# Performance work log

Measured on AMD Instinct MI355X. Metric: run time of the kernel, lower is better.

Reference implementation:

```python
import jax, jax.numpy as jnp
import numpy as np

DELTA_PULL = 0.5
DELTA_PUSH = 1.5
ALPHA, BETA, GAMMA = 1.0, 1.0, 0.001
M, E = 2_000_000, 32
NUM_IDS = 65  # labels 0..64; 0 = background


def setup_inputs() -> dict:
    key = jax.random.key(0)
    k1, k2 = jax.random.split(key)
    embeddings = jax.random.normal(k1, (M, E), dtype=jnp.float32)
    instance_labels = jax.random.randint(k2, (M,), 0, NUM_IDS, dtype=jnp.int64)
    return {"embeddings": embeddings, "instance_labels": instance_labels}


def reference(embeddings, instance_labels):
    # Foreground mask; background (label 0) points are excluded from every term.
    fg = instance_labels > 0
    labels = jnp.where(fg, instance_labels, 0).astype(jnp.int32)
    w = fg.astype(embeddings.dtype)  # [M]

    # Per-instance means via one fused segment-sum (replaces Python loop over ids).
    sums = jax.ops.segment_sum(embeddings * w[:, None], labels, num_segments=NUM_IDS)  # [C+1,E]
    counts = jax.ops.segment_sum(w, labels, num_segments=NUM_IDS)                       # [C+1]
    present = (counts > 0).at[0].set(False)  # slot 0 is background
    safe_counts = jnp.maximum(counts, 1.0)
    means = sums / safe_counts[:, None]  # [C+1,E]
    C = jnp.sum(present)
    Cf = jnp.maximum(C, 1).astype(embeddings.dtype)

    # Pull loss: per-point distance to own instance mean, hinged, per-instance mean, then mean over instances.
    diff_pt = embeddings - means[labels]
    d2_pt = jnp.sum(diff_pt * diff_pt, axis=1)
    dist_pt = jnp.sqrt(jnp.where(d2_pt > 0, d2_pt, 1.0))
    dist_pt = jnp.where(d2_pt > 0, dist_pt, 0.0)
    pull_pt = jnp.maximum(dist_pt - DELTA_PULL, 0.0) ** 2 * w
    pull_per_inst = jax.ops.segment_sum(pull_pt, labels, num_segments=NUM_IDS) / safe_counts
    pull_loss = jnp.sum(jnp.where(present, pull_per_inst, 0.0)) / Cf

    # Push loss: vectorized O(C^2) pairwise mean distances with upper-triangular mask.
    dm = means[:, None, :] - means[None, :, :]           # [C+1,C+1,E]
    d2 = jnp.sum(dm * dm, axis=-1)                        # [C+1,C+1]
    iu = jnp.triu(jnp.ones((NUM_IDS, NUM_IDS), bool), k=1)
    pairmask = iu & present[:, None] & present[None, :]
    pd = jnp.sqrt(jnp.where(pairmask, d2, 1.0))
    push = jnp.where(pairmask, jnp.maximum(2.0 * DELTA_PUSH - pd, 0.0) ** 2, 0.0)
    n_pairs = jnp.sum(pairmask)
    push_loss = jnp.where(
        n_pairs > 0,
        jnp.sum(push) / jnp.maximum(n_pairs, 1).astype(embeddings.dtype),
        0.0,
    )

    # Regularizer: mean norm of present instance means.
    mn2 = jnp.sum(means * means, axis=-1)
    mnorm = jnp.sqrt(jnp.where(present, mn2, 1.0))
    reg_loss = jnp.sum(jnp.where(present, mnorm, 0.0)) / Cf

    total = ALPHA * pull_loss + BETA * push_loss + GAMMA * reg_loss
    # If there are no foreground points, loss is 0 (matches torch early-return).
    total = jnp.where(C > 0, total, 0.0)
    return total
```

## Files before the change

### kernel.cpp

```cpp
#include <hip/hip_runtime.h>

#define NUM_IDS 65
#define EDIM 32
#define NSUM (NUM_IDS * EDIM)
#define NTOT (NSUM + NUM_IDS)
#define LPAD 33
#define R36 36
#define CP (NUM_IDS * R36)

#define WS_MEANS   0
#define WS_COEF    2080
#define WS_SUMS    2145
#define WS_PUSH    4290
#define WS_REG     4291
#define WS_CF      4292
#define WS_C       4293
#define WS_PULLACC 4294
#define WS_PART    4352

__global__ void k0_zero(float* __restrict__ ws) {
    int i = blockIdx.x * 256 + threadIdx.x;
    if (i < NTOT) ws[WS_SUMS + i] = 0.f;
}

__global__ __launch_bounds__(256) void k1_reduce(const float4* __restrict__ emb4,
                                                 const int* __restrict__ lab,
                                                 float* __restrict__ ws,
                                                 int M, int nb1, int atomic_mode) {
    __shared__ float ls[4 * CP];
    const int t = threadIdx.x;
    const int wave = t >> 6, lane = t & 63;
    const int s = lane >> 3;
    const int c = lane & 7;
    float* my = ls + wave * CP;
    for (int j = t; j < 4 * CP; j += 256) ls[j] = 0.f;
    __syncthreads();

    float cntreg = 0.f;
    const int lp1 = lane + 1;

    const long stride = (long)nb1 * 32;
    const long p0 = (long)blockIdx.x * 32 + wave * 8 + s;

    auto LD = [&](long p, int& L, float4& v) {
        if (p < M) { L = lab[p]; v = emb4[p * 8 + c]; }
        else       { L = 0; v = make_float4(0.f, 0.f, 0.f, 0.f); }
    };

    auto PR = [&](int L, float4 v) {
        const int off = L * R36 + 4 * c;
        float4 old = *(float4*)(my + off);
        const bool act = (L > 0);
        int key = act ? L : (-64 - s);
        int q0 = __shfl(key, 0 + c),  q1 = __shfl(key, 8 + c);
        int q2 = __shfl(key, 16 + c), q3 = __shfl(key, 24 + c);
        int q4 = __shfl(key, 32 + c), q5 = __shfl(key, 40 + c);
        int q6 = __shfl(key, 48 + c), q7 = __shfl(key, 56 + c);
        cntreg += (float)((q0 == lp1) + (q1 == lp1) + (q2 == lp1) + (q3 == lp1) +
                          (q4 == lp1) + (q5 == lp1) + (q6 == lp1) + (q7 == lp1));
        int ne = 0;
        ne += (0 < s && q0 == key); ne += (1 < s && q1 == key);
        ne += (2 < s && q2 == key); ne += (3 < s && q3 == key);
        ne += (4 < s && q4 == key); ne += (5 < s && q5 == key);
        ne += (6 < s && q6 == key);
        if (act && ne == 0) {
            float4 nv; nv.x = old.x + v.x; nv.y = old.y + v.y;
            nv.z = old.z + v.z; nv.w = old.w + v.w;
            *(float4*)(my + off) = nv;
        }
        if (__ballot(act && ne > 0)) {
            #pragma unroll 1
            for (int r = 1; r < 8; ++r) {
                if (!__ballot(act && ne == r)) break;
                if (act && ne == r) {
                    float4 o2 = *(float4*)(my + off);
                    o2.x += v.x; o2.y += v.y; o2.z += v.z; o2.w += v.w;
                    *(float4*)(my + off) = o2;
                }
            }
        }
    };

    int La, Lb; float4 va, vb;
    long pA = p0;
    LD(pA, La, va);
    while (pA < M) {
        const long pB = pA + stride;
        LD(pB, Lb, vb);
        PR(La, va);
        const long pA2 = pB + stride;
        LD(pA2, La, va);
        PR(Lb, vb);
        pA = pA2;
    }

    my[lp1 * R36 + 32] += cntreg;
    __syncthreads();

    for (int j = t; j < NTOT; j += 256) {
        int off = (j < NSUM) ? ((j >> 5) * R36 + (j & 31))
                             : ((j - NSUM) * R36 + 32);
        float v = ls[off] + ls[CP + off] + ls[2 * CP + off] + ls[3 * CP + off];
        if (atomic_mode) {
            if (v != 0.f) atomicAdd(&ws[WS_SUMS + j], v);
        } else {
            ws[WS_PART + (size_t)blockIdx.x * NTOT + j] = v;
        }
    }
}

__global__ __launch_bounds__(256) void k2_reduce_partials(float* __restrict__ ws, int nb1) {
    const int t = threadIdx.x;
    const int jl = t & 31, bl = t >> 5;
    const int j = blockIdx.x * 32 + jl;
    const float* part = ws + WS_PART;
    float acc = 0.f;
    if (j < NTOT)
        for (int b = bl; b < nb1; b += 8) acc += part[(size_t)b * NTOT + j];
    __shared__ float red[256];
    red[t] = acc;
    __syncthreads();
    for (int sd = 128; sd >= 32; sd >>= 1) {
        if (t < sd) red[t] += red[t + sd];
        __syncthreads();
    }
    if (t < 32) {
        int jj = blockIdx.x * 32 + t;
        if (jj < NTOT) ws[WS_SUMS + jj] = red[t];
    }
}

__global__ __launch_bounds__(256) void k3_finalize(float* __restrict__ ws) {
    __shared__ float lmean[NUM_IDS * LPAD];
    __shared__ float lcnt[NUM_IDS];
    __shared__ int   lpres[NUM_IDS];
    __shared__ float red[256];
    __shared__ float red2[256];
    const int t = threadIdx.x;
    const float* sg = ws + WS_SUMS;

    if (t < NUM_IDS) {
        float cv = sg[NSUM + t];
        lcnt[t] = cv;
        lpres[t] = (t > 0 && cv > 0.f) ? 1 : 0;
    }
    __syncthreads();

    for (int j = t; j < NSUM; j += 256) {
        int cc = j >> 5, e = j & 31;
        float m = sg[j] / fmaxf(lcnt[cc], 1.f);
        ws[WS_MEANS + j] = m;
        lmean[cc * LPAD + e] = m;
    }
    if (t < NUM_IDS) ws[WS_COEF + t] = lpres[t] ? (1.f / fmaxf(lcnt[t], 1.f)) : 0.f;
    __syncthreads();

    float psum = 0.f;
    for (int pi = t; pi < 2080; pi += 256) {
        int i = 0, rem = pi;
        while (rem >= NUM_IDS - 1 - i) { rem -= NUM_IDS - 1 - i; ++i; }
        int jj = i + 1 + rem;
        if (lpres[i] && lpres[jj]) {
            float d2 = 0.f;
            #pragma unroll
            for (int e = 0; e < EDIM; ++e) {
                float d = lmean[i * LPAD + e] - lmean[jj * LPAD + e];
                d2 += d * d;
            }
            float pd = sqrtf(d2);
            float h = fmaxf(3.0f - pd, 0.f);
            psum += h * h;
        }
    }
    float rsum = 0.f;
    if (t < NUM_IDS && lpres[t]) {
        float m2 = 0.f;
        #pragma unroll
        for (int e = 0; e < EDIM; ++e) { float m = lmean[t * LPAD + e]; m2 += m * m; }
        rsum = sqrtf(m2);
    }
    red[t] = psum; red2[t] = rsum;
    __syncthreads();
    for (int sd = 128; sd > 0; sd >>= 1) {
        if (t < sd) { red[t] += red[t + sd]; red2[t] += red2[t + sd]; }
        __syncthreads();
    }
    if (t == 0) {
        int C = 0;
        for (int cc = 1; cc < NUM_IDS; ++cc) C += lpres[cc];
        float Cf = fmaxf((float)C, 1.f);
        long np = (long)C * (C - 1) / 2;
        ws[WS_PUSH] = (np > 0) ? red[0] / (float)np : 0.f;
        ws[WS_REG]  = red2[0] / Cf;
        ws[WS_CF]   = Cf;
        ws[WS_C]    = (float)C;
        ws[WS_PULLACC] = 0.f;
    }
}

__global__ __launch_bounds__(256) void k4_pull(const float4* __restrict__ emb4,
                                               const int* __restrict__ lab,
                                               float* __restrict__ ws,
                                               int M, int nb4) {
    __shared__ float lmean[NUM_IDS * LPAD];
    __shared__ float lcoef[NUM_IDS];
    __shared__ float lpull[NUM_IDS];
    __shared__ float red[NUM_IDS];
    const int t = threadIdx.x;
    for (int j = t; j < NSUM; j += 256) lmean[(j >> 5) * LPAD + (j & 31)] = ws[WS_MEANS + j];
    if (t < NUM_IDS) { lcoef[t] = ws[WS_COEF + t]; lpull[t] = 0.f; }
    __syncthreads();

    const int c = t & 7;
    const long stride = (long)nb4 * 32;
    const long start = (long)blockIdx.x * 32 + (t >> 3);

    auto LD = [&](long p, int& L, float4& v) {
        if (p < M) { L = lab[p]; v = emb4[p * 8 + c]; }
        else       { L = 0; v = make_float4(0.f, 0.f, 0.f, 0.f); }
    };
    auto PR = [&](int L, float4 v) {
        float d2 = 0.f;
        if (L > 0) {
            int bse = L * LPAD + c * 4;
            float dx = v.x - lmean[bse + 0];
            float dy = v.y - lmean[bse + 1];
            float dz = v.z - lmean[bse + 2];
            float dw = v.w - lmean[bse + 3];
            d2 = dx * dx + dy * dy + dz * dz + dw * dw;
        }
        d2 += __shfl_xor(d2, 1);
        d2 += __shfl_xor(d2, 2);
        d2 += __shfl_xor(d2, 4);
        if (c == 0 && L > 0 && d2 > 0.f) {
            float dist = sqrtf(d2);
            float h = fmaxf(dist - 0.5f, 0.f);
            atomicAdd(&lpull[L], h * h);
        }
    };

    int L0, L1;
    float4 v0, v1;
    long pA = start;
    LD(pA, L0, v0);
    while (pA < M) {
        const long pB = pA + stride;
        LD(pB, L1, v1);
        PR(L0, v0);
        const long pA2 = pB + stride;
        LD(pA2, L0, v0);
        PR(L1, v1);
        pA = pA2;
    }
    __syncthreads();
    if (t < NUM_IDS) red[t] = lpull[t] * lcoef[t];
    __syncthreads();
    if (t == 0) {
        float sacc = 0.f;
        for (int cc = 1; cc < NUM_IDS; ++cc) sacc += red[cc];
        atomicAdd(&ws[WS_PULLACC], sacc);
    }
}

__global__ void k5_final(const float* __restrict__ ws, float* __restrict__ out) {
    if (threadIdx.x == 0) {
        float C = ws[WS_C];
        float total = 0.f;
        if (C > 0.f) {
            total = ws[WS_PULLACC] / ws[WS_CF]
                  + ws[WS_PUSH]
                  + 0.001f * ws[WS_REG];
        }
        out[0] = total;
    }
}

extern "C" void kernel_launch(void* const* d_in, const int* in_sizes, int n_in,
                              void* d_out, int out_size, void* d_ws, size_t ws_size,
                              hipStream_t stream) {
    const float4* emb4 = (const float4*)d_in[0];
    const int* lab = (const int*)d_in[1];
    float* ws = (float*)d_ws;
    float* out = (float*)d_out;
    const int M = in_sizes[1];

    long ws_floats = (long)(ws_size / 4);
    long avail = ws_floats - WS_PART - 64;
    int nb1 = (int)(avail / NTOT);
    if (nb1 > 1024) nb1 = 1024;
    int atomic_mode = (nb1 < 8) ? 1 : 0;
    if (atomic_mode) {
        nb1 = 1024;
        k0_zero<<<dim3(9), dim3(256), 0, stream>>>(ws);
    }

    k1_reduce<<<dim3(nb1), dim3(256), 0, stream>>>(emb4, lab, ws, M, nb1, atomic_mode);
    if (!atomic_mode)
        k2_reduce_partials<<<dim3((NTOT + 31) / 32), dim3(256), 0, stream>>>(ws, nb1);
    k3_finalize<<<dim3(1), dim3(256), 0, stream>>>(ws);
    const int nb4 = 2048;
    k4_pull<<<dim3(nb4), dim3(256), 0, stream>>>(emb4, lab, ws, M, nb4);
    k5_final<<<dim3(1), dim3(64), 0, stream>>>(ws, out);
}
```

Before: 169.0 us.

## Triple-buffer loads with inline asm and replace shuffles with DPP in both passes

Both streaming kernels replace the double-buffered load loop with a three-deep software pipeline. Loads are issued as inline-asm global loads with clamped addresses, and explicit vmcnt waits keep several memory requests in flight. The lane layout in the reduce kernel is transposed so the 8 points that collide sit within a DPP row, letting DPP permutes replace ds_bpermute shuffles for duplicate detection and counting. The pull kernel also uses DPP for its 8-lane reduction and float4 mean reads. This risks correctness in the hand-built DPP patterns and vmcnt assumptions, and reads clamped tail elements that are then masked out.

```diff
diff --git a/kernel.cpp b/kernel.cpp
--- a/kernel.cpp
+++ b/kernel.cpp
@@ -18,6 +18,23 @@
 #define WS_PULLACC 4294
 #define WS_PART    4352
 
+#define DPPI(x, ctrl) __builtin_amdgcn_update_dpp(0, (x), (ctrl), 0xF, 0xF, true)
+
+__device__ __forceinline__ void gload4(const float4* p, float4& d) {
+    asm volatile("global_load_dwordx4 %0, %1, off" : "=v"(d) : "v"(p));
+}
+__device__ __forceinline__ void gload1(const int* p, int& d) {
+    asm volatile("global_load_dword %0, %1, off" : "=v"(d) : "v"(p));
+}
+__device__ __forceinline__ void waitN() {
+    asm volatile("s_waitcnt vmcnt(4)" ::: "memory");
+    __builtin_amdgcn_sched_barrier(0);
+}
+__device__ __forceinline__ void wait0() {
+    asm volatile("s_waitcnt vmcnt(0)" ::: "memory");
+    __builtin_amdgcn_sched_barrier(0);
+}
+
 __global__ void k0_zero(float* __restrict__ ws) {
     int i = blockIdx.x * 256 + threadIdx.x;
     if (i < NTOT) ws[WS_SUMS + i] = 0.f;
@@ -26,75 +43,76 @@
 __global__ __launch_bounds__(256) void k1_reduce(const float4* __restrict__ emb4,
                                                  const int* __restrict__ lab,
                                                  float* __restrict__ ws,
-                                                 int M, int nb1, int atomic_mode) {
+                                                 int M, int nb1, int nit, int atomic_mode) {
     __shared__ float ls[4 * CP];
     const int t = threadIdx.x;
     const int wave = t >> 6, lane = t & 63;
-    const int s = lane >> 3;
-    const int c = lane & 7;
+    const int s = lane & 7;
+    const int c = lane >> 3;
     float* my = ls + wave * CP;
     for (int j = t; j < 4 * CP; j += 256) ls[j] = 0.f;
     __syncthreads();
 
-    float cntreg = 0.f;
+    const long Mm1 = (long)M - 1;
+    const long STR = (long)nb1 * 32;
+    const long p0 = (long)blockIdx.x * 32 + wave * 8 + s;
     const int lp1 = lane + 1;
-
-    const long stride = (long)nb1 * 32;
-    const long p0 = (long)blockIdx.x * 32 + wave * 8 + s;
-
-    auto LD = [&](long p, int& L, float4& v) {
-        if (p < M) { L = lab[p]; v = emb4[p * 8 + c]; }
-        else       { L = 0; v = make_float4(0.f, 0.f, 0.f, 0.f); }
+    int cntreg = 0;
+    const int negkey = -64 - s;
+    const int e1 = (s ^ 1) < s, e2 = (s ^ 2) < s, e3 = (s ^ 3) < s,
+              e4 = (s ^ 4) < s, e5 = (s ^ 5) < s, e6 = (s ^ 6) < s, e7 = (s ^ 7) < s;
+
+    auto ISSUE = [&](int j, int& L, float4& v) {
+        long p = p0 + (long)j * STR;
+        long pc = p < Mm1 ? p : Mm1;
+        gload1(lab + pc, L);
+        gload4(emb4 + pc * 8 + c, v);
     };
-
-    auto PR = [&](int L, float4 v) {
-        const int off = L * R36 + 4 * c;
-        float4 old = *(float4*)(my + off);
-        const bool act = (L > 0);
-        int key = act ? L : (-64 - s);
-        int q0 = __shfl(key, 0 + c),  q1 = __shfl(key, 8 + c);
-        int q2 = __shfl(key, 16 + c), q3 = __shfl(key, 24 + c);
-        int q4 = __shfl(key, 32 + c), q5 = __shfl(key, 40 + c);
-        int q6 = __shfl(key, 48 + c), q7 = __shfl(key, 56 + c);
-        cntreg += (float)((q0 == lp1) + (q1 == lp1) + (q2 == lp1) + (q3 == lp1) +
-                          (q4 == lp1) + (q5 == lp1) + (q6 == lp1) + (q7 == lp1));
-        int ne = 0;
-        ne += (0 < s && q0 == key); ne += (1 < s && q1 == key);
-        ne += (2 < s && q2 == key); ne += (3 < s && q3 == key);
-        ne += (4 < s && q4 == key); ne += (5 < s && q5 == key);
-        ne += (6 < s && q6 == key);
+    auto PROC = [&](int j, int L, float4 v) {
+        const bool inb = (p0 + (long)j * STR) < (long)M;
+        const bool act = inb && (L > 0);
+        int x0 = act ? L : negkey;
+        int x1 = DPPI(x0, 0xB1);
+        int x2 = DPPI(x0, 0x4E);
+        int x3 = DPPI(x1, 0x4E);
+        int x4 = DPPI(x0, 0x124);
+        int x5 = DPPI(x1, 0x124);
+        int x6 = DPPI(x2, 0x124);
+        int x7 = DPPI(x3, 0x124);
+        cntreg += (x0 == lp1) + (x1 == lp1) + (x2 == lp1) + (x3 == lp1)
+                + (x4 == lp1) + (x5 == lp1) + (x6 == lp1) + (x7 == lp1);
+        int ne = (e1 & (x1 == x0)) + (e2 & (x2 == x0)) + (e3 & (x3 == x0))
+               + (e4 & (x4 == x0)) + (e5 & (x5 == x0)) + (e6 & (x6 == x0))
+               + (e7 & (x7 == x0));
+        const int off = (act ? L : 0) * R36 + c * 4;
         if (act && ne == 0) {
-            float4 nv; nv.x = old.x + v.x; nv.y = old.y + v.y;
-            nv.z = old.z + v.z; nv.w = old.w + v.w;
-            *(float4*)(my + off) = nv;
+            float4 o = *(float4*)(my + off);
+            o.x += v.x; o.y += v.y; o.z += v.z; o.w += v.w;
+            *(float4*)(my + off) = o;
         }
         if (__ballot(act && ne > 0)) {
             #pragma unroll 1
             for (int r = 1; r < 8; ++r) {
                 if (!__ballot(act && ne == r)) break;
                 if (act && ne == r) {
-                    float4 o2 = *(float4*)(my + off);
-                    o2.x += v.x; o2.y += v.y; o2.z += v.z; o2.w += v.w;
-                    *(float4*)(my + off) = o2;
+                    float4 o = *(float4*)(my + off);
+                    o.x += v.x; o.y += v.y; o.z += v.z; o.w += v.w;
+                    *(float4*)(my + off) = o;
                 }
             }
         }
     };
 
-    int La, Lb; float4 va, vb;
-    long pA = p0;
-    LD(pA, La, va);
-    while (pA < M) {
-        const long pB = pA + stride;
-        LD(pB, Lb, vb);
-        PR(La, va);
-        const long pA2 = pB + stride;
-        LD(pA2, La, va);
-        PR(Lb, vb);
-        pA = pA2;
-    }
-
-    my[lp1 * R36 + 32] += cntreg;
+    int LA, LB, LC; float4 VA, VB, VC;
+    ISSUE(0, LA, VA); ISSUE(1, LB, VB);
+    for (int i = 0; i < nit; i += 3) {
+        ISSUE(i + 2, LC, VC); waitN(); PROC(i, LA, VA);
+        ISSUE(i + 3, LA, VA); waitN(); PROC(i + 1, LB, VB);
+        ISSUE(i + 4, LB, VB); waitN(); PROC(i + 2, LC, VC);
+    }
+    wait0();
+
+    my[lp1 * R36 + 32] += (float)cntreg;
     __syncthreads();
 
     for (int j = t; j < NTOT; j += 256) {
@@ -201,57 +219,54 @@
 __global__ __launch_bounds__(256) void k4_pull(const float4* __restrict__ emb4,
                                                const int* __restrict__ lab,
                                                float* __restrict__ ws,
-                                               int M, int nb4) {
-    __shared__ float lmean[NUM_IDS * LPAD];
+                                               int M, int nb4, int nit) {
+    __shared__ float lmean[NUM_IDS * R36];
     __shared__ float lcoef[NUM_IDS];
     __shared__ float lpull[NUM_IDS];
     __shared__ float red[NUM_IDS];
     const int t = threadIdx.x;
-    for (int j = t; j < NSUM; j += 256) lmean[(j >> 5) * LPAD + (j & 31)] = ws[WS_MEANS + j];
+    const int lane = t & 63;
+    const int s = lane >> 3, c = lane & 7;
+    for (int j = t; j < NSUM; j += 256) lmean[(j >> 5) * R36 + (j & 31)] = ws[WS_MEANS + j];
     if (t < NUM_IDS) { lcoef[t] = ws[WS_COEF + t]; lpull[t] = 0.f; }
     __syncthreads();
 
-    const int c = t & 7;
-    const long stride = (long)nb4 * 32;
-    const long start = (long)blockIdx.x * 32 + (t >> 3);
-
-    auto LD = [&](long p, int& L, float4& v) {
-        if (p < M) { L = lab[p]; v = emb4[p * 8 + c]; }
-        else       { L = 0; v = make_float4(0.f, 0.f, 0.f, 0.f); }
+    const long Mm1 = (long)M - 1;
+    const long STR = (long)nb4 * 32;
+    const long p0 = (long)blockIdx.x * 32 + (t >> 6) * 8 + s;
+
+    auto ISSUE = [&](int j, int& L, float4& v) {
+        long p = p0 + (long)j * STR;
+        long pc = p < Mm1 ? p : Mm1;
+        gload1(lab + pc, L);
+        gload4(emb4 + pc * 8 + c, v);
     };
-    auto PR = [&](int L, float4 v) {
-        float d2 = 0.f;
-        if (L > 0) {
-            int bse = L * LPAD + c * 4;
-            float dx = v.x - lmean[bse + 0];
-            float dy = v.y - lmean[bse + 1];
-            float dz = v.z - lmean[bse + 2];
-            float dw = v.w - lmean[bse + 3];
-            d2 = dx * dx + dy * dy + dz * dz + dw * dw;
-        }
-        d2 += __shfl_xor(d2, 1);
-        d2 += __shfl_xor(d2, 2);
-        d2 += __shfl_xor(d2, 4);
-        if (c == 0 && L > 0 && d2 > 0.f) {
+    auto PROC = [&](int j, int L, float4 v) {
+        const bool inb = (p0 + (long)j * STR) < (long)M;
+        const bool act = inb && (L > 0);
+        const float4 mu = *(const float4*)(lmean + L * R36 + c * 4);
+        float dx = v.x - mu.x, dy = v.y - mu.y, dz = v.z - mu.z, dw = v.w - mu.w;
+        float d2 = act ? (dx * dx + dy * dy + dz * dz + dw * dw) : 0.f;
+        int bb;
+        bb = DPPI(__float_as_int(d2), 0xB1); d2 += __int_as_float(bb);
+        bb = DPPI(__float_as_int(d2), 0x4E); d2 += __int_as_float(bb);
+        bb = DPPI(DPPI(__float_as_int(d2), 0x141), 0x1B);
+        d2 += __int_as_float(bb);
+        if (c == 0 && act && d2 > 0.f) {
             float dist = sqrtf(d2);
             float h = fmaxf(dist - 0.5f, 0.f);
             atomicAdd(&lpull[L], h * h);
         }
     };
 
-    int L0, L1;
-    float4 v0, v1;
-    long pA = start;
-    LD(pA, L0, v0);
-    while (pA < M) {
-        const long pB = pA + stride;
-        LD(pB, L1, v1);
-        PR(L0, v0);
-        const long pA2 = pB + stride;
-        LD(pA2, L0, v0);
-        PR(L1, v1);
-        pA = pA2;
-    }
+    int LA, LB, LC; float4 VA, VB, VC;
+    ISSUE(0, LA, VA); ISSUE(1, LB, VB);
+    for (int i = 0; i < nit; i += 3) {
+        ISSUE(i + 2, LC, VC); waitN(); PROC(i, LA, VA);
+        ISSUE(i + 3, LA, VA); waitN(); PROC(i + 1, LB, VB);
+        ISSUE(i + 4, LB, VB); waitN(); PROC(i + 2, LC, VC);
+    }
+    wait0();
     __syncthreads();
     if (t < NUM_IDS) red[t] = lpull[t] * lcoef[t];
     __syncthreads();
@@ -293,12 +308,19 @@
         nb1 = 1024;
         k0_zero<<<dim3(9), dim3(256), 0, stream>>>(ws);
     }
-
-    k1_reduce<<<dim3(nb1), dim3(256), 0, stream>>>(emb4, lab, ws, M, nb1, atomic_mode);
+    long str1 = (long)nb1 * 32;
+    int nit1 = (int)((M + str1 - 1) / str1);
+    nit1 = ((nit1 + 2) / 3) * 3;
+
+    const int nb4 = 2048;
+    long str4 = (long)nb4 * 32;
+    int nit4 = (int)((M + str4 - 1) / str4);
+    nit4 = ((nit4 + 2) / 3) * 3;
+
+    k1_reduce<<<dim3(nb1), dim3(256), 0, stream>>>(emb4, lab, ws, M, nb1, nit1, atomic_mode);
     if (!atomic_mode)
         k2_reduce_partials<<<dim3((NTOT + 31) / 32), dim3(256), 0, stream>>>(ws, nb1);
     k3_finalize<<<dim3(1), dim3(256), 0, stream>>>(ws);
-    const int nb4 = 2048;
-    k4_pull<<<dim3(nb4), dim3(256), 0, stream>>>(emb4, lab, ws, M, nb4);
+    k4_pull<<<dim3(nb4), dim3(256), 0, stream>>>(emb4, lab, ws, M, nb4, nit4);
     k5_final<<<dim3(1), dim3(64), 0, stream>>>(ws, out);
 }
```

Result: faster. 164.0 us (-3.0%).
